# Optimization experiments

Hardware: AMD Instinct MI355X
Metric: run time of the kernel (lower is better)

Reference implementation:

```python
import jax, jax.numpy as jnp
import numpy as np

N = 10000      # nodes
E = 160000     # edges (avg degree 16)
H = 128        # hidden_dim
L = 4          # propagation_depth
G = 64         # graphs in batch
ATOM_V = 119
BOND_V = 5
AVG_D_LOG = 1.0
EPS_SCALE = 1e-8


def setup_inputs() -> dict:
    key = jax.random.key(0)
    ks = jax.random.split(key, 12)
    x = jax.random.randint(ks[0], (N,), 0, ATOM_V)
    edge_index = jax.random.randint(ks[1], (2, E), 0, N)
    edge_attr = jax.random.randint(ks[2], (E,), 0, BOND_V)
    batch = jnp.sort(jax.random.randint(ks[3], (N,), 0, G))
    atom_emb = jax.random.normal(ks[4], (ATOM_V, H), jnp.float32) * 0.1
    bond_emb = jax.random.normal(ks[5], (BOND_V, H), jnp.float32) * 0.1
    pre_W = jax.random.normal(ks[6], (L, 3 * H, H), jnp.float32) / np.sqrt(3 * H)
    pre_b = jnp.zeros((L, H), jnp.float32)
    post_W = jax.random.normal(ks[7], (L, 10 * H, H), jnp.float32) / np.sqrt(10 * H)
    post_b = jnp.zeros((L, H), jnp.float32)
    out_W1 = jax.random.normal(ks[8], (3 * H, H), jnp.float32) / np.sqrt(3 * H)
    out_b1 = jnp.zeros((H,), jnp.float32)
    out_W2 = jax.random.normal(ks[9], (H, 1), jnp.float32) / np.sqrt(H)
    out_b2 = jnp.zeros((1,), jnp.float32)
    return {"x": x, "edge_index": edge_index, "edge_attr": edge_attr, "batch": batch,
            "atom_emb": atom_emb, "bond_emb": bond_emb,
            "pre_W": pre_W, "pre_b": pre_b, "post_W": post_W, "post_b": post_b,
            "out_W1": out_W1, "out_b1": out_b1, "out_W2": out_W2, "out_b2": out_b2}


def _seg_mean_sum_max(v, idx, num_seg, cnt):
    s = jax.ops.segment_sum(v, idx, num_segments=num_seg)
    mean = s / jnp.maximum(cnt, 1.0)[:, None]
    mx = jax.ops.segment_max(v, idx, num_segments=num_seg)
    mx = jnp.where(cnt[:, None] > 0, mx, 0.0)  # empty segments -> 0 (torch scatter)
    return mean, s, mx


def _clean(a):
    return jnp.where(jnp.isnan(a) | jnp.isinf(a), 0.0, a)


def reference(x, edge_index, edge_attr, batch, atom_emb, bond_emb,
              pre_W, pre_b, post_W, post_b, out_W1, out_b1, out_W2, out_b2):
    h = atom_emb[x]            # [N, H] atom encoder
    e = bond_emb[edge_attr]    # [E, H] bond encoder
    row, col = edge_index[0], edge_index[1]
    n = h.shape[0]
    deg = jax.ops.segment_sum(jnp.ones_like(col, jnp.float32), col, num_segments=n)
    D = deg[:, None]
    logD = jnp.log(D + 1.0)
    amp_fac = logD / AVG_D_LOG                       # amplification scaler
    att_fac = AVG_D_LOG / jnp.maximum(logD, EPS_SCALE)  # attenuation scaler
    n_layers = pre_W.shape[0]
    for l in range(n_layers):
        h_in = h
        z2 = jnp.concatenate([h[row], h[col], e], axis=-1)         # [E, 3H]
        msg = z2 @ pre_W[l] + pre_b[l]                             # pretrans (1 layer, no act)
        mean, s, mx = _seg_mean_sum_max(msg, col, n, deg)
        hagg = jnp.concatenate([mean, s, mx], axis=-1)             # [N, 3H]
        hcat = jnp.concatenate([hagg, hagg * amp_fac, hagg * att_fac, h_in], axis=-1)  # [N, 10H]
        h = hcat @ post_W[l] + post_b[l]                           # posttrans (1 layer)
        h = h + h_in                                               # residual
    # readout over graphs
    cnt = jax.ops.segment_sum(jnp.ones((n,), jnp.float32), batch, num_segments=G)
    rmean, rsum, rmax = _seg_mean_sum_max(h, batch, G, cnt)
    r = _clean(jnp.concatenate([rmean, rsum, rmax], axis=-1))      # [G, 3H]
    out = jax.nn.relu(r @ out_W1 + out_b1) @ out_W2 + out_b2       # [G, 1]
    return _clean(out)
```

## Files before the change

kernel.cpp:

```cpp
#include <hip/hip_runtime.h>
#include <hip/hip_bf16.h>
#include <math.h>

#define NN 10000
#define NE 160000
#define HD 128
#define NL 4
#define NG 64
#define NBLK 625
#define SMEM_BYTES 19584

typedef __attribute__((ext_vector_type(8))) short bf16x8;
typedef __attribute__((ext_vector_type(4))) short bf16x4;
typedef __attribute__((ext_vector_type(4))) float f32x4;

static __device__ __forceinline__ short f2bf(float f) {
    unsigned u = __float_as_uint(f);
    unsigned r = (u + 0x7FFFu + ((u >> 16) & 1u)) >> 16;
    return (short)r;
}
static __device__ __forceinline__ float bf2f(short s) {
    return __uint_as_float(((unsigned)(unsigned short)s) << 16);
}

__global__ void setup1_kernel(const int* __restrict__ x, const float* __restrict__ atom_emb,
                              float* __restrict__ h, float* __restrict__ deg,
                              int* __restrict__ cursor) {
    int idx = blockIdx.x * 256 + threadIdx.x;
    if (idx < NN) { deg[idx] = 0.f; cursor[idx] = 0; }
    if (idx < NN * HD) {
        int n = idx >> 7, f = idx & 127;
        h[idx] = atom_emb[x[n] * HD + f];
    }
}

__global__ __launch_bounds__(256) void setup2_kernel(
    const int* __restrict__ col, float* __restrict__ deg,
    const float* __restrict__ bond_emb,
    const float* __restrict__ pre_W, const float* __restrict__ pre_b,
    const float* __restrict__ post_W,
    float* __restrict__ btab, short* __restrict__ pre_Wt, short* __restrict__ post_Wt) {
    int b = blockIdx.x;
    if (b < 625) {
        int e = b * 256 + threadIdx.x;
        if (e < NE) atomicAdd(&deg[col[e]], 1.f);
        return;
    }
    if (b < 645) {
        int lb = b - 625;
        if (threadIdx.x < 128) {
            int l = lb / 5, bb = lb % 5;
            int f = threadIdx.x;
            const float* W2 = pre_W + (size_t)l * 384 * HD + 256 * HD;
            const float* eb = bond_emb + bb * HD;
            float acc = pre_b[l * HD + f];
            for (int k = 0; k < HD; ++k) acc = fmaf(eb[k], W2[k * HD + f], acc);
            btab[(l * 5 + bb) * HD + f] = acc;
        }
        return;
    }
    int idx = (b - 645) * 256 + threadIdx.x;
    if (idx < NL * 4 * 256 * 32) {
        int l = idx >> 15;
        int r = idx & 32767;
        int kblk = r >> 13;
        int rr = r & 8191;
        int j = rr >> 5, k = rr & 31;
        const float* Wl = pre_W + (size_t)l * 384 * HD;
        float v = (j < 128) ? Wl[(kblk * 32 + k) * HD + j]
                            : Wl[(128 + kblk * 32 + k) * HD + (j - 128)];
        pre_Wt[idx] = f2bf(v);
    }
    if (idx < NL * 40 * 128 * 32) {
        int l = idx / 163840;
        int r = idx % 163840;
        int kblk = r >> 12;
        int rr = r & 4095;
        int j = rr >> 5, k = rr & 31;
        post_Wt[idx] = f2bf(post_W[(size_t)l * 163840 + (size_t)(kblk * 32 + k) * HD + j]);
    }
}

__global__ __launch_bounds__(1024) void scan_facs_kernel(const float* __restrict__ deg,
                                                         int* __restrict__ offsets,
                                                         float* __restrict__ amp,
                                                         float* __restrict__ att) {
    __shared__ int s[1024];
    int t = threadIdx.x;
    int base = t * 10;
    int v[10];
    int lsum = 0;
    #pragma unroll
    for (int i = 0; i < 10; ++i) {
        int idx = base + i;
        int d = (idx < NN) ? (int)deg[idx] : 0;
        v[i] = d;
        lsum += d;
        if (idx < NN) {
            float logD = logf((float)d + 1.f);
            amp[idx] = logD;
            att[idx] = 1.f / fmaxf(logD, 1e-8f);
        }
    }
    s[t] = lsum;
    __syncthreads();
    for (int off = 1; off < 1024; off <<= 1) {
        int x2 = (t >= off) ? s[t - off] : 0;
        __syncthreads();
        s[t] += x2;
        __syncthreads();
    }
    int run = s[t] - lsum;
    #pragma unroll
    for (int i = 0; i < 10; ++i) {
        int idx = base + i;
        if (idx < NN) offsets[idx] = run;
        run += v[i];
    }
    if (t == 1023) offsets[NN] = run;
}

__global__ void scatter_kernel(const int* __restrict__ row, const int* __restrict__ col,
                               const int* __restrict__ ea, const int* __restrict__ offsets,
                               int* __restrict__ cursor, int* __restrict__ perm) {
    int e = blockIdx.x * 256 + threadIdx.x;
    if (e < NE) {
        int c = col[e];
        int pos = offsets[c] + atomicAdd(&cursor[c], 1);
        perm[pos] = row[e] | (ea[e] << 14);
    }
}

__global__ __launch_bounds__(256, 4) void pre_gemm_kernel(const float* __restrict__ h,
                                                          const short* __restrict__ Wt,
                                                          short* __restrict__ hw0,
                                                          float* __restrict__ hw1) {
    __shared__ short Ap[16][136];
    int t = threadIdx.x;
    int nb = blockIdx.x * 16;
    {
        int nl = t >> 4, f = (t & 15) * 8;
        int n = nb + nl;
        const float* src = h + (size_t)n * HD + f;
        float4 x0 = *(const float4*)src, x1 = *(const float4*)(src + 4);
        bf16x8 pk;
        pk[0]=f2bf(x0.x); pk[1]=f2bf(x0.y); pk[2]=f2bf(x0.z); pk[3]=f2bf(x0.w);
        pk[4]=f2bf(x1.x); pk[5]=f2bf(x1.y); pk[6]=f2bf(x1.z); pk[7]=f2bf(x1.w);
        *(bf16x8*)&Ap[nl][f] = pk;
    }
    __syncthreads();
    int wave = t >> 6, lane = t & 63;
    int lx = lane & 15, kb = lane >> 4;
    f32x4 acc[4];
    #pragma unroll
    for (int j = 0; j < 4; ++j) acc[j] = (f32x4){0.f, 0.f, 0.f, 0.f};
    #pragma unroll
    for (int ks = 0; ks < 4; ++ks) {
        bf16x8 a = *(const bf16x8*)&Ap[lx][ks * 32 + kb * 8];
        const short* bp = Wt + (size_t)ks * 8192 + (size_t)(wave * 64 + lx) * 32 + kb * 8;
        #pragma unroll
        for (int jj = 0; jj < 4; ++jj) {
            bf16x8 bfr = *(const bf16x8*)(bp + jj * 512);
            acc[jj] = __builtin_amdgcn_mfma_f32_16x16x32_bf16(a, bfr, acc[jj], 0, 0, 0);
        }
    }
    #pragma unroll
    for (int jj = 0; jj < 4; ++jj) {
        int c = wave * 64 + jj * 16 + lx;
        #pragma unroll
        for (int r_ = 0; r_ < 4; ++r_) {
            int n2 = nb + kb * 4 + r_;
            if (c < 128) hw0[(size_t)n2 * HD + c] = f2bf(acc[jj][r_]);
            else         hw1[(size_t)n2 * HD + (c - 128)] = acc[jj][r_];
        }
    }
}

__global__ __launch_bounds__(256, 4) void fused_kernel(
    const short* __restrict__ hw0_in, const float* __restrict__ hw1_in,
    const float* __restrict__ btabL,
    const int* __restrict__ offsets, const int* __restrict__ perm,
    const float* __restrict__ curH,
    const float* __restrict__ amp, const float* __restrict__ att,
    const short* __restrict__ Wt , const float* __restrict__ bias,
    float* __restrict__ nxtH,
    const short* __restrict__ nextWt, short* __restrict__ hw0o, float* __restrict__ hw1o) {
    __shared__ __align__(16) char smem[SMEM_BYTES];
    short (*aggB)[3][132] = (short(*)[3][132])smem;
    float (*btab_s)[128]  = (float(*)[128])(smem + 12672);
    short (*Ap2)[136]     = (short(*)[136])(smem + 15232);
    int t = threadIdx.x;
    int nb = blockIdx.x * 16;

    if (t < 160) {
        int bb = t >> 5, f4 = (t & 31) * 4;
        *(f32x4*)&btab_s[bb][f4] = *(const f32x4*)(btabL + bb * HD + f4);
    }
    __syncthreads();

    {
        int nl = t >> 4;
        int n = nb + nl;
        int f = (t & 15) * 8;
        int s0 = offsets[n];
        int d = offsets[n + 1] - s0;
        f32x4 sum0 = {0.f,0.f,0.f,0.f}, sum1 = {0.f,0.f,0.f,0.f};
        f32x4 mx0 = {-INFINITY,-INFINITY,-INFINITY,-INFINITY};
        f32x4 mx1 = mx0;
        int i = 0;
        for (; i + 4 <= d; i += 4) {
            int p0 = perm[s0 + i],     p1 = perm[s0 + i + 1];
            int p2 = perm[s0 + i + 2], p3 = perm[s0 + i + 3];
            bf16x8 a0 = *(const bf16x8*)(hw0_in + (size_t)(p0 & 16383) * HD + f);
            bf16x8 a1 = *(const bf16x8*)(hw0_in + (size_t)(p1 & 16383) * HD + f);
            bf16x8 a2 = *(const bf16x8*)(hw0_in + (size_t)(p2 & 16383) * HD + f);
            bf16x8 a3 = *(const bf16x8*)(hw0_in + (size_t)(p3 & 16383) * HD + f);
            const float* t0 = &btab_s[p0 >> 14][f];
            const float* t1 = &btab_s[p1 >> 14][f];
            const float* t2 = &btab_s[p2 >> 14][f];
            const float* t3 = &btab_s[p3 >> 14][f];
            #pragma unroll
            for (int q = 0; q < 4; ++q) {
                float v00 = bf2f(a0[q]) + t0[q];
                float v01 = bf2f(a0[q+4]) + t0[q+4];
                float v10 = bf2f(a1[q]) + t1[q];
                float v11 = bf2f(a1[q+4]) + t1[q+4];
                float v20 = bf2f(a2[q]) + t2[q];
                float v21 = bf2f(a2[q+4]) + t2[q+4];
                float v30 = bf2f(a3[q]) + t3[q];
                float v31 = bf2f(a3[q+4]) + t3[q+4];
                sum0[q] += (v00 + v10) + (v20 + v30);
                sum1[q] += (v01 + v11) + (v21 + v31);
                mx0[q] = fmaxf(fmaxf(fmaxf(mx0[q], v00), fmaxf(v10, v20)), v30);
                mx1[q] = fmaxf(fmaxf(fmaxf(mx1[q], v01), fmaxf(v11, v21)), v31);
            }
        }
        for (; i < d; ++i) {
            int p0 = perm[s0 + i];
            bf16x8 a0 = *(const bf16x8*)(hw0_in + (size_t)(p0 & 16383) * HD + f);
            const float* t0 = &btab_s[p0 >> 14][f];
            #pragma unroll
            for (int q = 0; q < 4; ++q) {
                float v00 = bf2f(a0[q]) + t0[q];
                float v01 = bf2f(a0[q+4]) + t0[q+4];
                sum0[q] += v00; sum1[q] += v01;
                mx0[q] = fmaxf(mx0[q], v00);
                mx1[q] = fmaxf(mx1[q], v01);
            }
        }
        const float* cp = hw1_in + (size_t)n * HD + f;
        f32x4 c0 = *(const f32x4*)cp, c1 = *(const f32x4*)(cp + 4);
        f32x4 me0, me1, so0, so1, mo0, mo1;
        if (d > 0) {
            float df = (float)d, di = 1.f / df;
            so0 = sum0 + df * c0;  so1 = sum1 + df * c1;
            me0 = sum0 * di + c0;  me1 = sum1 * di + c1;
            mo0 = mx0 + c0;        mo1 = mx1 + c1;
        } else {
            me0 = (f32x4){0.f,0.f,0.f,0.f}; me1 = me0;
            so0 = me0; so1 = me0; mo0 = me0; mo1 = me0;
        }
        bf16x8 pk;
        #pragma unroll
        for (int q = 0; q < 4; ++q) { pk[q] = f2bf(me0[q]); pk[q+4] = f2bf(me1[q]); }
        *(bf16x8*)&aggB[nl][0][f] = pk;
        #pragma unroll
        for (int q = 0; q < 4; ++q) { pk[q] = f2bf(so0[q]); pk[q+4] = f2bf(so1[q]); }
        *(bf16x8*)&aggB[nl][1][f] = pk;
        #pragma unroll
        for (int q = 0; q < 4; ++q) { pk[q] = f2bf(mo0[q]); pk[q+4] = f2bf(mo1[q]); }
        *(bf16x8*)&aggB[nl][2][f] = pk;
    }
    __syncthreads();

    int wave = t >> 6, lane = t & 63;
    int lx = lane & 15, kb = lane >> 4;
    int n_lx = nb + lx;
    float famp = amp[n_lx], fatt = att[n_lx];
    const float* hsrc = curH + (size_t)n_lx * HD;
    const short* bbase = Wt + (size_t)(wave * 32 + lx) * 32 + kb * 8;
    f32x4 acc0 = {0.f,0.f,0.f,0.f}, acc1 = acc0;
    #pragma unroll
    for (int ks = 0; ks < 40; ++ks) {
        constexpr int KS4096 = 4096;
        int r = ks >> 2;
        int kk = (ks & 3) * 32 + kb * 8;
        bf16x8 afrag;
        if (r < 9) {
            int ag = r % 3, fi = r / 3;
            bf16x8 raw = *(const bf16x8*)&aggB[lx][ag][kk];
            if (fi == 0) afrag = raw;
            else {
                float fac = (fi == 1) ? famp : fatt;
                #pragma unroll
                for (int q = 0; q < 8; ++q) afrag[q] = f2bf(bf2f(raw[q]) * fac);
            }
        } else {
            const float* src = hsrc + kk;
            float4 x0 = *(const float4*)src, x1 = *(const float4*)(src + 4);
            afrag[0]=f2bf(x0.x); afrag[1]=f2bf(x0.y); afrag[2]=f2bf(x0.z); afrag[3]=f2bf(x0.w);
            afrag[4]=f2bf(x1.x); afrag[5]=f2bf(x1.y); afrag[6]=f2bf(x1.z); afrag[7]=f2bf(x1.w);
        }
        const short* bp = bbase + (size_t)ks * KS4096;
        bf16x8 b0 = *(const bf16x8*)bp;
        bf16x8 b1 = *(const bf16x8*)(bp + 512);
        acc0 = __builtin_amdgcn_mfma_f32_16x16x32_bf16(afrag, b0, acc0, 0, 0, 0);
        acc1 = __builtin_amdgcn_mfma_f32_16x16x32_bf16(afrag, b1, acc1, 0, 0, 0);
    }
    #pragma unroll
    for (int jj = 0; jj < 2; ++jj) {
        int c = wave * 32 + jj * 16 + lx;
        float bc = bias[c];
        f32x4 av = jj ? acc1 : acc0;
        #pragma unroll
        for (int r_ = 0; r_ < 4; ++r_) {
            int n2 = nb + kb * 4 + r_;
            size_t off = (size_t)n2 * HD + c;
            float ho = av[r_] + bc + curH[off];
            nxtH[off] = ho;
            Ap2[n2 - nb][c] = f2bf(ho);
        }
    }
    if (nextWt != nullptr) {
        __syncthreads();
        f32x4 acc[4];
        #pragma unroll
        for (int j = 0; j < 4; ++j) acc[j] = (f32x4){0.f, 0.f, 0.f, 0.f};
        #pragma unroll
        for (int ks = 0; ks < 4; ++ks) {
            bf16x8 aa = *(const bf16x8*)&Ap2[lx][ks * 32 + kb * 8];
            const short* bp = nextWt + (size_t)ks * 8192 + (size_t)(wave * 64 + lx) * 32 + kb * 8;
            #pragma unroll
            for (int jj = 0; jj < 4; ++jj) {
                bf16x8 bfr = *(const bf16x8*)(bp + jj * 512);
                acc[jj] = __builtin_amdgcn_mfma_f32_16x16x32_bf16(aa, bfr, acc[jj], 0, 0, 0);
            }
        }
        #pragma unroll
        for (int jj = 0; jj < 4; ++jj) {
            int c = wave * 64 + jj * 16 + lx;
            #pragma unroll
            for (int r_ = 0; r_ < 4; ++r_) {
                int n2 = nb + kb * 4 + r_;
                if (c < 128) hw0o[(size_t)n2 * HD + c] = f2bf(acc[jj][r_]);
                else         hw1o[(size_t)n2 * HD + (c - 128)] = acc[jj][r_];
            }
        }
    }
}

__global__ __launch_bounds__(256) void pool_out_kernel(
    const float* __restrict__ h, const int* __restrict__ batch,
    const float* __restrict__ W1, const float* __restrict__ b1,
    const float* __restrict__ W2, const float* __restrict__ b2,
    float* __restrict__ out)
{
    __shared__ float rs[384];
    __shared__ float red[256];
    __shared__ float s2[128], m2[128];
    int g = blockIdx.x, t = threadIdx.x;
    int lo = 0, hi = NN;
    while (lo < hi) { int mid = (lo + hi) >> 1; if (batch[mid] < g) lo = mid + 1; else hi = mid; }
    int lo2 = lo, hi2 = NN;
    while (lo2 < hi2) { int mid = (lo2 + hi2) >> 1; if (batch[mid] < g + 1) lo2 = mid + 1; else hi2 = mid; }
    int cnt = lo2 - lo;
    int f = t & 127, grp = t >> 7;
    float sum = 0.f, mx = -INFINITY;
    for (int n = lo + grp; n < lo2; n += 2) {
        float v = h[(size_t)n * HD + f];
        sum += v; mx = fmaxf(mx, v);
    }
    if (grp == 1) { s2[f] = sum; m2[f] = mx; }
    __syncthreads();
    if (grp == 0) {
        sum += s2[f]; mx = fmaxf(mx, m2[f]);
        float mean = (cnt > 0) ? sum / (float)cnt : 0.f;
        float so = (cnt > 0) ? sum : 0.f;
        float mo = (cnt > 0) ? mx : 0.f;
        if (isnan(mean) || isinf(mean)) mean = 0.f;
        if (isnan(so) || isinf(so)) so = 0.f;
        if (isnan(mo) || isinf(mo)) mo = 0.f;
        rs[f] = mean; rs[128 + f] = so; rs[256 + f] = mo;
    }
    __syncthreads();
    {
        int j = t & 127, kh = t >> 7;
        float acc = 0.f;
        for (int k = kh * 192; k < kh * 192 + 192; ++k)
            acc = fmaf(rs[k], W1[k * HD + j], acc);
        red[t] = acc;
    }
    __syncthreads();
    if (t < 128) {
        float v = fmaxf(red[t] + red[128 + t] + b1[t], 0.f);
        red[t] = v * W2[t];
    }
    __syncthreads();
    for (int s = 64; s > 0; s >>= 1) {
        if (t < s) red[t] += red[t + s];
        __syncthreads();
    }
    if (t == 0) {
        float o = red[0] + b2[0];
        if (isnan(o) || isinf(o)) o = 0.f;
        out[g] = o;
    }
}

extern "C" void kernel_launch(void* const* d_in, const int* in_sizes, int n_in,
                              void* d_out, int out_size, void* d_ws, size_t ws_size,
                              hipStream_t stream)
{
    const int* x          = (const int*)d_in[0];
    const int* ei         = (const int*)d_in[1];
    const int* ea         = (const int*)d_in[2];
    const int* batch      = (const int*)d_in[3];
    const float* atom_emb = (const float*)d_in[4];
    const float* bond_emb = (const float*)d_in[5];
    const float* pre_W    = (const float*)d_in[6];
    const float* pre_b    = (const float*)d_in[7];
    const float* post_W   = (const float*)d_in[8];
    const float* post_b   = (const float*)d_in[9];
    const float* out_W1   = (const float*)d_in[10];
    const float* out_b1   = (const float*)d_in[11];
    const float* out_W2   = (const float*)d_in[12];
    const float* out_b2   = (const float*)d_in[13];
    float* out = (float*)d_out;
    const int* row = ei;
    const int* col = ei + NE;

    char* p = (char*)d_ws;
    auto alloc = [&](size_t bytes) { char* r = p; p += (bytes + 255) & ~(size_t)255; return r; };
    float*    deg     = (float*)alloc((size_t)NN * 4);
    float*    amp     = (float*)alloc((size_t)NN * 4);
    float*    att     = (float*)alloc((size_t)NN * 4);
    int*      offsets = (int*)alloc((size_t)(NN + 1) * 4);
    int*      cursor  = (int*)alloc((size_t)NN * 4);
    int*      perm    = (int*)alloc((size_t)NE * 4);
    float*    hA      = (float*)alloc((size_t)NN * HD * 4);
    float*    hB      = (float*)alloc((size_t)NN * HD * 4);
    short*    hw0A    = (short*)alloc((size_t)NN * HD * 2);
    short*    hw0B    = (short*)alloc((size_t)NN * HD * 2);
    float*    hw1A    = (float*)alloc((size_t)NN * HD * 4);
    float*    hw1B    = (float*)alloc((size_t)NN * HD * 4);
    float*    btab    = (float*)alloc((size_t)NL * 5 * HD * 4);
    short*    pre_Wt  = (short*)alloc((size_t)NL * 4 * 256 * 32 * 2);
    short*    post_Wt = (short*)alloc((size_t)NL * 40 * 128 * 32 * 2);

    setup1_kernel<<<(NN * HD) / 256, 256, 0, stream>>>(x, atom_emb, hA, deg, cursor);
    setup2_kernel<<<645 + (NL * 40 * 128 * 32 + 255) / 256, 256, 0, stream>>>(
        col, deg, bond_emb, pre_W, pre_b, post_W, btab, pre_Wt, post_Wt);
    scan_facs_kernel<<<1, 1024, 0, stream>>>(deg, offsets, amp, att);
    scatter_kernel<<<(NE + 255) / 256, 256, 0, stream>>>(row, col, ea, offsets, cursor, perm);
    pre_gemm_kernel<<<NBLK, 256, 0, stream>>>(hA, pre_Wt, hw0A, hw1A);

    float* curH = hA;
    float* nxtH = hB;
    const short* hw0_in = hw0A;
    const float* hw1_in = hw1A;
    for (int l = 0; l < NL; ++l) {
        short* hw0_out = (l & 1) ? hw0A : hw0B;
        float* hw1_out = (l & 1) ? hw1A : hw1B;
        const short* nextWt = (l + 1 < NL) ? (pre_Wt + (size_t)(l + 1) * 32768) : nullptr;
        fused_kernel<<<NBLK, 256, 0, stream>>>(
            hw0_in, hw1_in, btab + (size_t)l * 5 * HD, offsets, perm,
            curH, amp, att, post_Wt + (size_t)l * 163840,
            post_b + (size_t)l * HD, nxtH, nextWt, hw0_out, hw1_out);
        float* tmp = curH; curH = nxtH; nxtH = tmp;
        hw0_in = hw0_out; hw1_in = hw1_out;
    }

    pool_out_kernel<<<NG, 256, 0, stream>>>(curH, batch, out_W1, out_b1, out_W2, out_b2, out);
}
```

Baseline: 288.6 us.

## Transpose post weights via shared tile and double-buffer B-fragment loads in posttrans GEMM

The post_W bf16 conversion in setup moves to dedicated blocks that read rows coalesced into a shared-memory tile and write transposed 16-element vectors. This replaces a strided per-element gather and shrinks the setup grid to the pre_W portion only. In the fused kernel, the posttrans MFMA loop now prefetches the next group of four k-steps' weight fragments into alternating register buffers, overlapping global loads with MFMA work. This adds register pressure (16 extra bf16x8 vectors), which could lower occupancy.

After: 291.5 us. About the same (+1.0%).

```diff
diff --git a/kernel.cpp b/kernel.cpp
--- a/kernel.cpp
+++ b/kernel.cpp
@@ -41,25 +41,46 @@
     const float* __restrict__ post_W,
     float* __restrict__ btab, short* __restrict__ pre_Wt, short* __restrict__ post_Wt) {
     int b = blockIdx.x;
+    int t = threadIdx.x;
     if (b < 625) {
-        int e = b * 256 + threadIdx.x;
+        int e = b * 256 + t;
         if (e < NE) atomicAdd(&deg[col[e]], 1.f);
         return;
     }
     if (b < 645) {
         int lb = b - 625;
-        if (threadIdx.x < 128) {
+        if (t < 128) {
             int l = lb / 5, bb = lb % 5;
-            int f = threadIdx.x;
             const float* W2 = pre_W + (size_t)l * 384 * HD + 256 * HD;
             const float* eb = bond_emb + bb * HD;
-            float acc = pre_b[l * HD + f];
-            for (int k = 0; k < HD; ++k) acc = fmaf(eb[k], W2[k * HD + f], acc);
-            btab[(l * 5 + bb) * HD + f] = acc;
+            float acc = pre_b[l * HD + t];
+            for (int k = 0; k < HD; ++k) acc = fmaf(eb[k], W2[k * HD + t], acc);
+            btab[(l * 5 + bb) * HD + t] = acc;
         }
         return;
     }
-    int idx = (b - 645) * 256 + threadIdx.x;
+    if (b < 805) {
+        __shared__ short tile[32][136];
+        int tid = b - 645;
+        int l = tid / 40, kblk = tid % 40;
+        const float* src = post_W + (size_t)l * 163840 + (size_t)kblk * 32 * HD;
+        #pragma unroll
+        for (int i = 0; i < 16; ++i) {
+            int flat = i * 256 + t;
+            int k = flat >> 7, j = flat & 127;
+            tile[k][j] = f2bf(src[flat]);
+        }
+        __syncthreads();
+        short* dst = post_Wt + (size_t)(l * 40 + kblk) * 4096;
+        int j = t >> 1, k0 = (t & 1) * 16;
+        bf16x8 o0, o1;
+        #pragma unroll
+        for (int q = 0; q < 8; ++q) { o0[q] = tile[k0 + q][j]; o1[q] = tile[k0 + 8 + q][j]; }
+        *(bf16x8*)(dst + t * 16) = o0;
+        *(bf16x8*)(dst + t * 16 + 8) = o1;
+        return;
+    }
+    int idx = (b - 805) * 256 + t;
     if (idx < NL * 4 * 256 * 32) {
         int l = idx >> 15;
         int r = idx & 32767;
@@ -70,14 +91,6 @@
         float v = (j < 128) ? Wl[(kblk * 32 + k) * HD + j]
                             : Wl[(128 + kblk * 32 + k) * HD + (j - 128)];
         pre_Wt[idx] = f2bf(v);
-    }
-    if (idx < NL * 40 * 128 * 32) {
-        int l = idx / 163840;
-        int r = idx % 163840;
-        int kblk = r >> 12;
-        int rr = r & 4095;
-        int j = rr >> 5, k = rr & 31;
-        post_Wt[idx] = f2bf(post_W[(size_t)l * 163840 + (size_t)(kblk * 32 + k) * HD + j]);
     }
 }
 
@@ -280,32 +293,55 @@
     const float* hsrc = curH + (size_t)n_lx * HD;
     const short* bbase = Wt + (size_t)(wave * 32 + lx) * 32 + kb * 8;
     f32x4 acc0 = {0.f,0.f,0.f,0.f}, acc1 = acc0;
-    #pragma unroll
-    for (int ks = 0; ks < 40; ++ks) {
-        constexpr int KS4096 = 4096;
-        int r = ks >> 2;
-        int kk = (ks & 3) * 32 + kb * 8;
-        bf16x8 afrag;
-        if (r < 9) {
-            int ag = r % 3, fi = r / 3;
-            bf16x8 raw = *(const bf16x8*)&aggB[lx][ag][kk];
-            if (fi == 0) afrag = raw;
-            else {
-                float fac = (fi == 1) ? famp : fatt;
-                #pragma unroll
-                for (int q = 0; q < 8; ++q) afrag[q] = f2bf(bf2f(raw[q]) * fac);
+
+    bf16x8 bufE[8], bufO[8];
+    #pragma unroll
+    for (int u = 0; u < 4; ++u) {
+        const short* bp = bbase + (size_t)u * 4096;
+        bufE[u * 2]     = *(const bf16x8*)bp;
+        bufE[u * 2 + 1] = *(const bf16x8*)(bp + 512);
+    }
+    #pragma unroll
+    for (int g = 0; g < 10; ++g) {
+        if (g + 1 < 10) {
+            #pragma unroll
+            for (int u = 0; u < 4; ++u) {
+                const short* bp = bbase + (size_t)((g + 1) * 4 + u) * 4096;
+                if (g & 1) {
+                    bufE[u * 2]     = *(const bf16x8*)bp;
+                    bufE[u * 2 + 1] = *(const bf16x8*)(bp + 512);
+                } else {
+                    bufO[u * 2]     = *(const bf16x8*)bp;
+                    bufO[u * 2 + 1] = *(const bf16x8*)(bp + 512);
+                }
             }
-        } else {
-            const float* src = hsrc + kk;
-            float4 x0 = *(const float4*)src, x1 = *(const float4*)(src + 4);
-            afrag[0]=f2bf(x0.x); afrag[1]=f2bf(x0.y); afrag[2]=f2bf(x0.z); afrag[3]=f2bf(x0.w);
-            afrag[4]=f2bf(x1.x); afrag[5]=f2bf(x1.y); afrag[6]=f2bf(x1.z); afrag[7]=f2bf(x1.w);
-        }
-        const short* bp = bbase + (size_t)ks * KS4096;
-        bf16x8 b0 = *(const bf16x8*)bp;
-        bf16x8 b1 = *(const bf16x8*)(bp + 512);
-        acc0 = __builtin_amdgcn_mfma_f32_16x16x32_bf16(afrag, b0, acc0, 0, 0, 0);
-        acc1 = __builtin_amdgcn_mfma_f32_16x16x32_bf16(afrag, b1, acc1, 0, 0, 0);
+        }
+        #pragma unroll
+        for (int u = 0; u < 4; ++u) {
+            int ks = g * 4 + u;
+            int r = ks >> 2;
+            int kk = (ks & 3) * 32 + kb * 8;
+            bf16x8 afrag;
+            if (r < 9) {
+                int ag = r % 3, fi = r / 3;
+                bf16x8 raw = *(const bf16x8*)&aggB[lx][ag][kk];
+                if (fi == 0) afrag = raw;
+                else {
+                    float fac = (fi == 1) ? famp : fatt;
+                    #pragma unroll
+                    for (int q = 0; q < 8; ++q) afrag[q] = f2bf(bf2f(raw[q]) * fac);
+                }
+            } else {
+                const float* src = hsrc + kk;
+                float4 x0 = *(const float4*)src, x1 = *(const float4*)(src + 4);
+                afrag[0]=f2bf(x0.x); afrag[1]=f2bf(x0.y); afrag[2]=f2bf(x0.z); afrag[3]=f2bf(x0.w);
+                afrag[4]=f2bf(x1.x); afrag[5]=f2bf(x1.y); afrag[6]=f2bf(x1.z); afrag[7]=f2bf(x1.w);
+            }
+            bf16x8 b0 = (g & 1) ? bufO[u * 2]     : bufE[u * 2];
+            bf16x8 b1 = (g & 1) ? bufO[u * 2 + 1] : bufE[u * 2 + 1];
+            acc0 = __builtin_amdgcn_mfma_f32_16x16x32_bf16(afrag, b0, acc0, 0, 0, 0);
+            acc1 = __builtin_amdgcn_mfma_f32_16x16x32_bf16(afrag, b1, acc1, 0, 0, 0);
+        }
     }
     #pragma unroll
     for (int jj = 0; jj < 2; ++jj) {
@@ -448,7 +484,7 @@
     short*    post_Wt = (short*)alloc((size_t)NL * 40 * 128 * 32 * 2);
 
     setup1_kernel<<<(NN * HD) / 256, 256, 0, stream>>>(x, atom_emb, hA, deg, cursor);
-    setup2_kernel<<<645 + (NL * 40 * 128 * 32 + 255) / 256, 256, 0, stream>>>(
+    setup2_kernel<<<805 + (NL * 4 * 256 * 32 + 255) / 256, 256, 0, stream>>>(
         col, deg, bond_emb, pre_W, pre_b, post_W, btab, pre_Wt, post_Wt);
     scan_facs_kernel<<<1, 1024, 0, stream>>>(deg, offsets, amp, att);
     scatter_kernel<<<(NE + 255) / 256, 256, 0, stream>>>(row, col, ea, offsets, cursor, perm);
```
